# Performance work log

Measured on AMD Instinct MI355X. Metric: run time of the kernel, lower is better.

The kernel has to match this reference:

```python
import jax, jax.numpy as jnp
import numpy as np

L, D, H, N = 9, 256, 4, 1024
DH = D // H          # head dim = 64
FH = DH // 2         # fourier half dim = 32


def _lin(x, W, b):
    return x @ W + b


def _ln(x, g, b, eps=1e-5):
    mu = jnp.mean(x, -1, keepdims=True)
    var = jnp.mean((x - mu) ** 2, -1, keepdims=True)
    return (x - mu) * jax.lax.rsqrt(var + eps) * g + b


def _ffn(x, m, W1, b1, g, beta, W2, b2):
    h = jax.nn.gelu(_ln(_lin(jnp.concatenate([x, m], -1), W1, b1), g, beta), approximate=False)
    return x + _lin(h, W2, b2)


def _rotate_half(x):
    x1, x2 = x[..., 0::2], x[..., 1::2]
    return jnp.stack((-x2, x1), -1).reshape(x.shape)


def _rope(f, t):
    return t * f[0] + _rotate_half(t) * f[1]


def _posenc(kpts, Wr):
    proj = kpts @ Wr                                   # [b,n,FH]
    emb = jnp.stack([jnp.cos(proj), jnp.sin(proj)], 0)  # [2,b,n,FH]
    emb = jnp.repeat(emb, 2, axis=3)                    # [2,b,n,DH]
    return emb[:, None]                                 # [2,1,b,n,DH]


def _heads(t):
    b, n, _ = t.shape
    return t.reshape(b, n, H, DH).transpose(0, 2, 1, 3)


def _merge(t):
    b, h, n, d = t.shape
    return t.transpose(0, 2, 1, 3).reshape(b, n, h * d)


def _self_block(x, enc, Wqkv, bqkv, Wo, bo, fp):
    b, n, _ = x.shape
    qkv = _lin(x, Wqkv, bqkv).reshape(b, n, H, DH, 3).transpose(0, 2, 1, 3, 4)
    q, k, v = qkv[..., 0], qkv[..., 1], qkv[..., 2]
    q, k = _rope(enc, q), _rope(enc, k)
    attn = jax.nn.softmax(jnp.einsum('bhid,bhjd->bhij', q, k) * DH ** -0.5, -1)
    msg = _lin(_merge(jnp.einsum('bhij,bhjd->bhid', attn, v)), Wo, bo)
    return _ffn(x, msg, *fp)


def _cross_block(x0, x1, Wqk, bqk, Wv, bv, Wo, bo, fp):
    s = DH ** -0.25
    qk0 = _heads(_lin(x0, Wqk, bqk)) * s
    qk1 = _heads(_lin(x1, Wqk, bqk)) * s
    v0, v1 = _heads(_lin(x0, Wv, bv)), _heads(_lin(x1, Wv, bv))
    sim = jnp.einsum('bhid,bhjd->bhij', qk0, qk1)       # shared similarity
    m0 = jnp.einsum('bhij,bhjd->bhid', jax.nn.softmax(sim, -1), v1)
    m1 = jnp.einsum('bhij,bhid->bhjd', jax.nn.softmax(sim, -2), v0)
    m0, m1 = _lin(_merge(m0), Wo, bo), _lin(_merge(m1), Wo, bo)
    return _ffn(x0, m0, *fp), _ffn(x1, m1, *fp)


def _assignment(d0, d1, Wp, bp, Wz, bz):
    s = D ** -0.25
    md0, md1 = _lin(d0, Wp, bp) * s, _lin(d1, Wp, bp) * s
    sim = jnp.einsum('bmd,bnd->bmn', md0, md1)
    z0 = d0 @ Wz + bz[:1]                               # [b,m,1]
    z1 = d1 @ Wz + bz[:1]                               # [b,n,1]
    cert = jax.nn.log_sigmoid(z0) + jnp.swapaxes(jax.nn.log_sigmoid(z1), 1, 2)
    inner = jax.nn.log_softmax(sim, -1) + jax.nn.log_softmax(sim, -2) + cert
    col = jax.nn.log_sigmoid(-z0)                       # [b,m,1]
    row = jnp.swapaxes(jax.nn.log_sigmoid(-z1), 1, 2)   # [b,1,n]
    top = jnp.concatenate([inner, col], 2)
    bot = jnp.concatenate([row, jnp.zeros_like(row[:, :, :1])], 2)
    return jnp.concatenate([top, bot], 1)               # [b,m+1,n+1]


def _forward(desc0, desc1, kpts0, kpts1, Wr,
             sWqkv, sbqkv, sWo, sbo, sfW1, sfb1, sfg, sfbeta, sfW2, sfb2,
             cWqk, cbqk, cWv, cbv, cWo, cbo, cfW1, cfb1, cfg, cfbeta, cfW2, cfb2,
             mWp, mbp, mWz, mbz):
    enc0, enc1 = _posenc(kpts0, Wr), _posenc(kpts1, Wr)
    for i in range(L):
        sfp = (sfW1[i], sfb1[i], sfg[i], sfbeta[i], sfW2[i], sfb2[i])
        cfp = (cfW1[i], cfb1[i], cfg[i], cfbeta[i], cfW2[i], cfb2[i])
        desc0 = _self_block(desc0, enc0, sWqkv[i], sbqkv[i], sWo[i], sbo[i], sfp)
        desc1 = _self_block(desc1, enc1, sWqkv[i], sbqkv[i], sWo[i], sbo[i], sfp)
        desc0, desc1 = _cross_block(desc0, desc1, cWqk[i], cbqk[i], cWv[i], cbv[i], cWo[i], cbo[i], cfp)
    return _assignment(desc0, desc1, mWp, mbp, mWz, mbz)


def setup_inputs() -> dict:
    key = jax.random.key(0)
    ks = iter(jax.random.split(key, 64))

    def nrm(shape, std=0.02):
        return std * jax.random.normal(next(ks), shape, jnp.float32)

    return {
        'desc0': nrm((1, N, D), 1.0), 'desc1': nrm((1, N, D), 1.0),
        'kpts0': nrm((1, N, 2), 1.0), 'kpts1': nrm((1, N, 2), 1.0),
        'Wr': nrm((2, FH), 1.0),
        'sWqkv': nrm((L, D, 3 * D)), 'sbqkv': jnp.zeros((L, 3 * D), jnp.float32),
        'sWo': nrm((L, D, D)), 'sbo': jnp.zeros((L, D), jnp.float32),
        'sfW1': nrm((L, 2 * D, 2 * D)), 'sfb1': jnp.zeros((L, 2 * D), jnp.float32),
        'sfg': jnp.ones((L, 2 * D), jnp.float32), 'sfbeta': jnp.zeros((L, 2 * D), jnp.float32),
        'sfW2': nrm((L, 2 * D, D)), 'sfb2': jnp.zeros((L, D), jnp.float32),
        'cWqk': nrm((L, D, D)), 'cbqk': jnp.zeros((L, D), jnp.float32),
        'cWv': nrm((L, D, D)), 'cbv': jnp.zeros((L, D), jnp.float32),
        'cWo': nrm((L, D, D)), 'cbo': jnp.zeros((L, D), jnp.float32),
        'cfW1': nrm((L, 2 * D, 2 * D)), 'cfb1': jnp.zeros((L, 2 * D), jnp.float32),
        'cfg': jnp.ones((L, 2 * D), jnp.float32), 'cfbeta': jnp.zeros((L, 2 * D), jnp.float32),
        'cfW2': nrm((L, 2 * D, D)), 'cfb2': jnp.zeros((L, D), jnp.float32),
        'mWp': nrm((D, D)), 'mbp': jnp.zeros((D,), jnp.float32),
        'mWz': nrm((D, 1)), 'mbz': jnp.zeros((D,), jnp.float32),
    }


def reference(desc0, desc1, kpts0, kpts1, Wr,
              sWqkv, sbqkv, sWo, sbo, sfW1, sfb1, sfg, sfbeta, sfW2, sfb2,
              cWqk, cbqk, cWv, cbv, cWo, cbo, cfW1, cfb1, cfg, cfbeta, cfW2, cfb2,
              mWp, mbp, mWz, mbz):
    return _forward(desc0, desc1, kpts0, kpts1, Wr,
                    sWqkv, sbqkv, sWo, sbo, sfW1, sfb1, sfg, sfbeta, sfW2, sfb2,
                    cWqk, cbqk, cWv, cbv, cWo, cbo, cfW1, cfb1, cfg, cfbeta, cfW2, cfb2,
                    mWp, mbp, mWz, mbz)
```

## Files before the change

kernel.cpp:

```cpp
#include <hip/hip_runtime.h>
#include <cmath>

#define NTOK 1024
#define DM   256
#define NH   4
#define DH   64
#define NL   9

typedef __attribute__((ext_vector_type(8))) __bf16 bf16x8;
typedef __attribute__((ext_vector_type(4))) __bf16 bf16x4;
typedef __attribute__((ext_vector_type(4))) float  f32x4;

__device__ __forceinline__ float logsigf(float x) {
    return fminf(x, 0.0f) - log1pf(expf(-fabsf(x)));
}

__device__ __forceinline__ __bf16 f2bf(float f) {
    unsigned u = __float_as_uint(f);
    u = (u + 0x7FFFu + ((u >> 16) & 1u)) >> 16;
    unsigned short s = (unsigned short)u;
    return __builtin_bit_cast(__bf16, s);
}

__global__ __launch_bounds__(256) void wtrans_all_k(
    const float* __restrict__ sWqkv, const float* __restrict__ sWo,
    const float* __restrict__ sfW1,  const float* __restrict__ sfW2,
    const float* __restrict__ cWqk,  const float* __restrict__ cWv,
    const float* __restrict__ cWo,   const float* __restrict__ cfW1,
    const float* __restrict__ cfW2,  const float* __restrict__ mWp,
    __bf16* __restrict__ wb)
{
    const int z = blockIdx.z;
    const float* src; __bf16* dst; int K, N, b;
    if      (z <  9) { src = sWqkv; dst = wb;            K = 256; N = 768; b = z;      }
    else if (z < 18) { src = sWo;   dst = wb + 1769472;  K = 256; N = 256; b = z - 9;  }
    else if (z < 27) { src = sfW1;  dst = wb + 2359296;  K = 512; N = 512; b = z - 18; }
    else if (z < 36) { src = sfW2;  dst = wb + 4718592;  K = 512; N = 256; b = z - 27; }
    else if (z < 45) { src = cWqk;  dst = wb + 5898240;  K = 256; N = 256; b = z - 36; }
    else if (z < 54) { src = cWv;   dst = wb + 6488064;  K = 256; N = 256; b = z - 45; }
    else if (z < 63) { src = cWo;   dst = wb + 7077888;  K = 256; N = 256; b = z - 54; }
    else if (z < 72) { src = cfW1;  dst = wb + 7667712;  K = 512; N = 512; b = z - 63; }
    else if (z < 81) { src = cfW2;  dst = wb + 10027008; K = 512; N = 256; b = z - 72; }
    else             { src = mWp;   dst = wb + 11206656; K = 256; N = 256; b = 0;      }
    const int n0 = blockIdx.x * 32, k0 = blockIdx.y * 32;
    if (n0 >= N || k0 >= K) return;
    src += (size_t)b * K * N;
    dst += (size_t)b * K * N;

    __shared__ __bf16 t[32][36];
    const int tx = threadIdx.x & 31, ty = threadIdx.x >> 5;
    #pragma unroll
    for (int i = 0; i < 4; ++i) {
        int k = ty + i * 8;
        t[tx][k] = f2bf(src[(size_t)(k0 + k) * N + n0 + tx]);
    }
    __syncthreads();
    const int nr = threadIdx.x >> 3, kc = (threadIdx.x & 7) * 4;
    bf16x4 v = *(const bf16x4*)&t[nr][kc];
    int outr = n0 + nr;
    if (z < 9) {
        int h = outr / 192, r = outr % 192;
        outr = (r % 3) * 256 + h * 64 + (r / 3);
    }
    *(bf16x4*)&dst[(size_t)outr * K + k0 + kc] = v;
}

__global__ __launch_bounds__(256) void wfuse_k(
    const __bf16* __restrict__ tW1s, const __bf16* __restrict__ tWos,
    const __bf16* __restrict__ tW1c, const __bf16* __restrict__ tWoc,
    __bf16* __restrict__ tW1f)
{
    const int z = blockIdx.z, bx = blockIdx.x, tid = threadIdx.x;
    const __bf16* A  = (z < 9) ? tW1s + (size_t)z * 262144 : tW1c + (size_t)(z - 9) * 262144;
    const __bf16* B  = (z < 9) ? tWos + (size_t)z * 65536  : tWoc + (size_t)(z - 9) * 65536;
    __bf16* dst      = tW1f + (size_t)z * 262144;
    const int row0 = blockIdx.y * 32;

    if (bx < 4) {
        const int row = tid >> 3, kc = (tid & 7) * 8;
        bf16x8 v = *(const bf16x8*)&A[(size_t)(row0 + row) * 512 + bx * 64 + kc];
        *(bf16x8*)&dst[(size_t)(row0 + row) * 512 + bx * 64 + kc] = v;
        return;
    }

    __shared__ __bf16 As[8][32][40];
    __shared__ __bf16 Bs[8][64][40];
    const int w = tid >> 6, l = tid & 63;
    const int col0 = (bx - 4) * 64;
    const int wr = (w >> 1) * 16, wc = (w & 1) * 32;
    f32x4 acc0 = {0.f, 0.f, 0.f, 0.f};
    f32x4 acc1 = {0.f, 0.f, 0.f, 0.f};

    const int ar = tid >> 3, ac = (tid & 7) * 4;
    const int tnr = tid >> 3, tkc = (tid & 7) * 8;

    #pragma unroll
    for (int c = 0; c < 8; ++c) {
        bf16x4 av = *(const bf16x4*)&A[(size_t)(row0 + ar) * 512 + 256 + c * 32 + ac];
        *(bf16x4*)&As[c][ar][ac] = av;
        bf16x8 bv = *(const bf16x8*)&B[(size_t)(c * 32 + tnr) * 256 + col0 + tkc];
        #pragma unroll
        for (int e = 0; e < 8; ++e) Bs[c][tkc + e][tnr] = bv[e];
    }
    __syncthreads();
    #pragma unroll
    for (int c = 0; c < 8; ++c) {
        bf16x8 af  = *(const bf16x8*)&As[c][wr + (l & 15)][(l >> 4) * 8];
        bf16x8 bf0 = *(const bf16x8*)&Bs[c][wc + (l & 15)][(l >> 4) * 8];
        bf16x8 bf1 = *(const bf16x8*)&Bs[c][wc + 16 + (l & 15)][(l >> 4) * 8];
        acc0 = __builtin_amdgcn_mfma_f32_16x16x32_bf16(af, bf0, acc0, 0, 0, 0);
        acc1 = __builtin_amdgcn_mfma_f32_16x16x32_bf16(af, bf1, acc1, 0, 0, 0);
    }
    #pragma unroll
    for (int t2 = 0; t2 < 2; ++t2) {
        f32x4 a = t2 ? acc1 : acc0;
        int cc = col0 + wc + t2 * 16 + (l & 15);
        #pragma unroll
        for (int rg = 0; rg < 4; ++rg) {
            int rr = row0 + wr + (l >> 4) * 4 + rg;
            dst[(size_t)rr * 512 + 256 + cc] = f2bf(a[rg]);
        }
    }
}

__global__ __launch_bounds__(256) void bfuse_k(
    const float* __restrict__ sbo, const float* __restrict__ sfW1,
    const float* __restrict__ sfb1, const float* __restrict__ cbo,
    const float* __restrict__ cfW1, const float* __restrict__ cfb1,
    float* __restrict__ bf)
{
    const int z = blockIdx.y;
    const float* bo = (z < 9) ? sbo + z * 256 : cbo + (z - 9) * 256;
    const float* W1 = (z < 9) ? sfW1 + (size_t)z * 262144 : cfW1 + (size_t)(z - 9) * 262144;
    const float* b1 = (z < 9) ? sfb1 + z * 512 : cfb1 + (z - 9) * 512;
    const int o = blockIdx.x * 256 + threadIdx.x;
    float acc = 0.f;
    for (int m = 0; m < 256; ++m)
        acc += bo[m] * W1[(size_t)(256 + m) * 512 + o];
    bf[(size_t)z * 512 + o] = b1[o] + acc;
}

__global__ __launch_bounds__(256) void gemm_qkv_k(
    const __bf16* __restrict__ Ab, const __bf16* __restrict__ Bt,
    const float* __restrict__ bias,
    const float* __restrict__ encc, const float* __restrict__ encs,
    __bf16* __restrict__ qh, __bf16* __restrict__ kh, __bf16* __restrict__ vh)
{
    __shared__ __bf16 As[8][32][40];
    __shared__ __bf16 Bs[8][64][40];
    const int tid = threadIdx.x;
    const int w = tid >> 6, l = tid & 63;
    const int row0 = blockIdx.y * 32, col0 = blockIdx.x * 64;
    const int wr = (w >> 1) * 16, wc = (w & 1) * 32;
    const int quad = l >> 4, l16 = l & 15;
    f32x4 acc0 = {0.f, 0.f, 0.f, 0.f};
    f32x4 acc1 = {0.f, 0.f, 0.f, 0.f};

    const int ar = tid >> 3, ac = (tid & 7) * 4;
    const int bnr = tid >> 2, bkc = (tid & 3) * 8;

    #pragma unroll
    for (int c = 0; c < 8; ++c) {
        const int k0 = c * 32;
        bf16x4 av = *(const bf16x4*)&Ab[(size_t)(row0 + ar) * 256 + k0 + ac];
        *(bf16x4*)&As[c][ar][ac] = av;
        bf16x8 bv = *(const bf16x8*)&Bt[(size_t)(col0 + bnr) * 256 + k0 + bkc];
        *(bf16x8*)&Bs[c][bnr][bkc] = bv;
    }
    __syncthreads();
    #pragma unroll
    for (int c = 0; c < 8; ++c) {
        bf16x8 af  = *(const bf16x8*)&As[c][wr + l16][quad * 8];
        bf16x8 bf0 = *(const bf16x8*)&Bs[c][wc + l16][quad * 8];
        bf16x8 bf1 = *(const bf16x8*)&Bs[c][wc + 16 + l16][quad * 8];
        acc0 = __builtin_amdgcn_mfma_f32_16x16x32_bf16(af, bf0, acc0, 0, 0, 0);
        acc1 = __builtin_amdgcn_mfma_f32_16x16x32_bf16(af, bf1, acc1, 0, 0, 0);
    }

    const int typ = col0 >> 8;
    const int hh  = (col0 & 255) >> 6;
    __bf16* dst = (typ == 0) ? qh : (typ == 1) ? kh : vh;
    #pragma unroll
    for (int t2 = 0; t2 < 2; ++t2) {
        f32x4 a = t2 ? acc1 : acc0;
        const int d = wc + t2 * 16 + l16;
        const float bvv = bias[hh * 192 + d * 3 + typ];
        float full[4], pair[4];
        #pragma unroll
        for (int rg = 0; rg < 4; ++rg) full[rg] = a[rg] + bvv;
        #pragma unroll
        for (int rg = 0; rg < 4; ++rg) pair[rg] = __shfl_xor(full[rg], 1);
        const float sgn = (d & 1) ? 1.0f : -1.0f;
        #pragma unroll
        for (int rg = 0; rg < 4; ++rg) {
            int rr = row0 + wr + quad * 4 + rg;
            float outv;
            if (typ == 2) {
                outv = full[rg];
            } else {
                float c = encc[(size_t)rr * 64 + d];
                float s = encs[(size_t)rr * 64 + d];
                outv = full[rg] * c + sgn * pair[rg] * s;
            }
            int im = rr >> 10, n = rr & 1023;
            dst[(((size_t)(im * 4 + hh)) * 1024 + n) * 64 + d] = f2bf(outv);
        }
    }
}

__global__ __launch_bounds__(256) void gemm_bf_k(
    const __bf16* __restrict__ Ab, const __bf16* __restrict__ A1b,
    const __bf16* __restrict__ Bt, const float* __restrict__ bias,
    float* __restrict__ C, int K, int Nn, int ldc, float scale)
{
    __shared__ __bf16 As[8][32][40];
    __shared__ __bf16 Bs[8][64][40];
    const int tid = threadIdx.x;
    const int w = tid >> 6, l = tid & 63;
    const int row0 = blockIdx.y * 32, col0 = blockIdx.x * 64;
    const int wr = (w >> 1) * 16, wc = (w & 1) * 32;
    f32x4 acc0 = {0.f, 0.f, 0.f, 0.f};
    f32x4 acc1 = {0.f, 0.f, 0.f, 0.f};

    const int ar = tid >> 3, ac = (tid & 7) * 4;
    const int bnr = tid >> 2, bkc = (tid & 3) * 8;

    for (int p0 = 0; p0 < K; p0 += 256) {
        #pragma unroll
        for (int c = 0; c < 8; ++c) {
            const int k0 = p0 + c * 32;
            const int kk = k0 + ac;
            const __bf16* src = (A1b && kk >= 256)
                ? &A1b[(size_t)(row0 + ar) * 256 + (kk - 256)]
                : &Ab[(size_t)(row0 + ar) * 256 + kk];
            bf16x4 av = *(const bf16x4*)src;
            *(bf16x4*)&As[c][ar][ac] = av;
            bf16x8 bv = *(const bf16x8*)&Bt[(size_t)(col0 + bnr) * K + k0 + bkc];
            *(bf16x8*)&Bs[c][bnr][bkc] = bv;
        }
        __syncthreads();
        #pragma unroll
        for (int c = 0; c < 8; ++c) {
            bf16x8 af  = *(const bf16x8*)&As[c][wr + (l & 15)][(l >> 4) * 8];
            bf16x8 bf0 = *(const bf16x8*)&Bs[c][wc + (l & 15)][(l >> 4) * 8];
            bf16x8 bf1 = *(const bf16x8*)&Bs[c][wc + 16 + (l & 15)][(l >> 4) * 8];
            acc0 = __builtin_amdgcn_mfma_f32_16x16x32_bf16(af, bf0, acc0, 0, 0, 0);
            acc1 = __builtin_amdgcn_mfma_f32_16x16x32_bf16(af, bf1, acc1, 0, 0, 0);
        }
        __syncthreads();
    }

    #pragma unroll
    for (int t2 = 0; t2 < 2; ++t2) {
        f32x4 a = t2 ? acc1 : acc0;
        int cc = col0 + wc + t2 * 16 + (l & 15);
        float bvv = bias ? bias[cc] : 0.0f;
        #pragma unroll
        for (int rg = 0; rg < 4; ++rg) {
            int rr = row0 + wr + (l >> 4) * 4 + rg;
            C[(size_t)rr * ldc + cc] = (a[rg] + bvv) * scale;
        }
    }
}

__global__ __launch_bounds__(256) void gemm_bfb_k(
    const __bf16* __restrict__ Ab, const __bf16* __restrict__ Bt,
    const float* __restrict__ bias, __bf16* __restrict__ Cb, float scale)
{
    __shared__ __bf16 As[8][32][40];
    __shared__ __bf16 Bs[8][64][40];
    const int tid = threadIdx.x;
    const int w = tid >> 6, l = tid & 63;
    const int row0 = blockIdx.y * 32, col0 = blockIdx.x * 64;
    const int wr = (w >> 1) * 16, wc = (w & 1) * 32;
    f32x4 acc0 = {0.f, 0.f, 0.f, 0.f};
    f32x4 acc1 = {0.f, 0.f, 0.f, 0.f};

    const int ar = tid >> 3, ac = (tid & 7) * 4;
    const int bnr = tid >> 2, bkc = (tid & 3) * 8;

    #pragma unroll
    for (int c = 0; c < 8; ++c) {
        const int k0 = c * 32;
        bf16x4 av = *(const bf16x4*)&Ab[(size_t)(row0 + ar) * 256 + k0 + ac];
        *(bf16x4*)&As[c][ar][ac] = av;
        bf16x8 bv = *(const bf16x8*)&Bt[(size_t)(col0 + bnr) * 256 + k0 + bkc];
        *(bf16x8*)&Bs[c][bnr][bkc] = bv;
    }
    __syncthreads();
    #pragma unroll
    for (int c = 0; c < 8; ++c) {
        bf16x8 af  = *(const bf16x8*)&As[c][wr + (l & 15)][(l >> 4) * 8];
        bf16x8 bf0 = *(const bf16x8*)&Bs[c][wc + (l & 15)][(l >> 4) * 8];
        bf16x8 bf1 = *(const bf16x8*)&Bs[c][wc + 16 + (l & 15)][(l >> 4) * 8];
        acc0 = __builtin_amdgcn_mfma_f32_16x16x32_bf16(af, bf0, acc0, 0, 0, 0);
        acc1 = __builtin_amdgcn_mfma_f32_16x16x32_bf16(af, bf1, acc1, 0, 0, 0);
    }

    #pragma unroll
    for (int t2 = 0; t2 < 2; ++t2) {
        f32x4 a = t2 ? acc1 : acc0;
        int cc = col0 + wc + t2 * 16 + (l & 15);
        float bvv = bias[cc];
        #pragma unroll
        for (int rg = 0; rg < 4; ++rg) {
            int rr = row0 + wr + (l >> 4) * 4 + rg;
            Cb[(size_t)rr * 256 + cc] = f2bf((a[rg] + bvv) * scale);
        }
    }
}

__global__ __launch_bounds__(256) void gemm_bfa_k(
    const __bf16* __restrict__ Ab, const __bf16* __restrict__ Bt,
    const float* __restrict__ bias, const float* __restrict__ R,
    float* __restrict__ C, __bf16* __restrict__ Cb, int Nn)
{
    __shared__ __bf16 As[8][32][40];
    __shared__ __bf16 Bs[8][64][40];
    const int tid = threadIdx.x;
    const int w = tid >> 6, l = tid & 63;
    const int row0 = blockIdx.y * 32, col0 = blockIdx.x * 64;
    const int wr = (w >> 1) * 16, wc = (w & 1) * 32;
    f32x4 acc0 = {0.f, 0.f, 0.f, 0.f};
    f32x4 acc1 = {0.f, 0.f, 0.f, 0.f};

    const int ar = tid >> 3, ac = (tid & 7) * 4;
    const int bnr = tid >> 2, bkc = (tid & 3) * 8;

    for (int p0 = 0; p0 < 512; p0 += 256) {
        #pragma unroll
        for (int c = 0; c < 8; ++c) {
            const int k0 = p0 + c * 32;
            bf16x4 av = *(const bf16x4*)&Ab[(size_t)(row0 + ar) * 512 + k0 + ac];
            *(bf16x4*)&As[c][ar][ac] = av;
            bf16x8 bv = *(const bf16x8*)&Bt[(size_t)(col0 + bnr) * 512 + k0 + bkc];
            *(bf16x8*)&Bs[c][bnr][bkc] = bv;
        }
        __syncthreads();
        #pragma unroll
        for (int c = 0; c < 8; ++c) {
            bf16x8 af  = *(const bf16x8*)&As[c][wr + (l & 15)][(l >> 4) * 8];
            bf16x8 bf0 = *(const bf16x8*)&Bs[c][wc + (l & 15)][(l >> 4) * 8];
            bf16x8 bf1 = *(const bf16x8*)&Bs[c][wc + 16 + (l & 15)][(l >> 4) * 8];
            acc0 = __builtin_amdgcn_mfma_f32_16x16x32_bf16(af, bf0, acc0, 0, 0, 0);
            acc1 = __builtin_amdgcn_mfma_f32_16x16x32_bf16(af, bf1, acc1, 0, 0, 0);
        }
        __syncthreads();
    }

    #pragma unroll
    for (int t2 = 0; t2 < 2; ++t2) {
        f32x4 a = t2 ? acc1 : acc0;
        int cc = col0 + wc + t2 * 16 + (l & 15);
        float bvv = bias[cc];
        #pragma unroll
        for (int rg = 0; rg < 4; ++rg) {
            int rr = row0 + wr + (l >> 4) * 4 + rg;
            float outv = a[rg] + bvv + R[(size_t)rr * Nn + cc];
            C[(size_t)rr * Nn + cc]  = outv;
            Cb[(size_t)rr * Nn + cc] = f2bf(outv);
        }
    }
}

__global__ __launch_bounds__(256) void gemm_hm2_k(
    const __bf16* __restrict__ Ab, const __bf16* __restrict__ Btq,
    const float* __restrict__ bq, const __bf16* __restrict__ Btv,
    const float* __restrict__ bv, __bf16* __restrict__ outq,
    __bf16* __restrict__ outv, float scaleq)
{
    const int bx = blockIdx.x;
    const __bf16* Bt  = (bx < 4) ? Btq : Btv;
    const float* bias = (bx < 4) ? bq : bv;
    __bf16* C         = (bx < 4) ? outq : outv;
    const float scale = (bx < 4) ? scaleq : 1.0f;

    __shared__ __bf16 As[8][32][40];
    __shared__ __bf16 Bs[8][64][40];
    const int tid = threadIdx.x;
    const int w = tid >> 6, l = tid & 63;
    const int row0 = blockIdx.y * 32, col0 = (bx & 3) * 64;
    const int wr = (w >> 1) * 16, wc = (w & 1) * 32;
    f32x4 acc0 = {0.f, 0.f, 0.f, 0.f};
    f32x4 acc1 = {0.f, 0.f, 0.f, 0.f};

    const int ar = tid >> 3, ac = (tid & 7) * 4;
    const int bnr = tid >> 2, bkc = (tid & 3) * 8;

    #pragma unroll
    for (int c = 0; c < 8; ++c) {
        const int k0 = c * 32;
        bf16x4 av = *(const bf16x4*)&Ab[(size_t)(row0 + ar) * 256 + k0 + ac];
        *(bf16x4*)&As[c][ar][ac] = av;
        bf16x8 bv8 = *(const bf16x8*)&Bt[(size_t)(col0 + bnr) * 256 + k0 + bkc];
        *(bf16x8*)&Bs[c][bnr][bkc] = bv8;
    }
    __syncthreads();
    #pragma unroll
    for (int c = 0; c < 8; ++c) {
        bf16x8 af  = *(const bf16x8*)&As[c][wr + (l & 15)][(l >> 4) * 8];
        bf16x8 bf0 = *(const bf16x8*)&Bs[c][wc + (l & 15)][(l >> 4) * 8];
        bf16x8 bf1 = *(const bf16x8*)&Bs[c][wc + 16 + (l & 15)][(l >> 4) * 8];
        acc0 = __builtin_amdgcn_mfma_f32_16x16x32_bf16(af, bf0, acc0, 0, 0, 0);
        acc1 = __builtin_amdgcn_mfma_f32_16x16x32_bf16(af, bf1, acc1, 0, 0, 0);
    }

    #pragma unroll
    for (int t2 = 0; t2 < 2; ++t2) {
        f32x4 a = t2 ? acc1 : acc0;
        int cc = col0 + wc + t2 * 16 + (l & 15);
        float bvv = bias ? bias[cc] : 0.0f;
        int h = cc >> 6, d = cc & 63;
        #pragma unroll
        for (int rg = 0; rg < 4; ++rg) {
            int rr = row0 + wr + (l >> 4) * 4 + rg;
            int im = rr >> 10, n = rr & 1023;
            C[(((size_t)(im * 4 + h)) * 1024 + n) * 64 + d] = f2bf((a[rg] + bvv) * scale);
        }
    }
}

__global__ __launch_bounds__(256) void gemm_bt_k(
    const __bf16* __restrict__ Ab, const __bf16* __restrict__ Bb,
    float* __restrict__ C, int Nn)
{
    __shared__ __bf16 As[8][32][40];
    __shared__ __bf16 Bs[8][64][40];
    const int tid = threadIdx.x;
    const int w = tid >> 6, l = tid & 63;
    const int row0 = blockIdx.y * 32, col0 = blockIdx.x * 64;
    const int wr = (w >> 1) * 16, wc = (w & 1) * 32;
    f32x4 acc0 = {0.f, 0.f, 0.f, 0.f};
    f32x4 acc1 = {0.f, 0.f, 0.f, 0.f};

    const int ar = tid >> 3, ac = (tid & 7) * 4;
    const int bnr = tid >> 2, bkc = (tid & 3) * 8;

    #pragma unroll
    for (int c = 0; c < 8; ++c) {
        const int k0 = c * 32;
        bf16x4 av = *(const bf16x4*)&Ab[(size_t)(row0 + ar) * 256 + k0 + ac];
        *(bf16x4*)&As[c][ar][ac] = av;
        bf16x8 bv = *(const bf16x8*)&Bb[(size_t)(col0 + bnr) * 256 + k0 + bkc];
        *(bf16x8*)&Bs[c][bnr][bkc] = bv;
    }
    __syncthreads();
    #pragma unroll
    for (int c = 0; c < 8; ++c) {
        bf16x8 af  = *(const bf16x8*)&As[c][wr + (l & 15)][(l >> 4) * 8];
        bf16x8 bf0 = *(const bf16x8*)&Bs[c][wc + (l & 15)][(l >> 4) * 8];
        bf16x8 bf1 = *(const bf16x8*)&Bs[c][wc + 16 + (l & 15)][(l >> 4) * 8];
        acc0 = __builtin_amdgcn_mfma_f32_16x16x32_bf16(af, bf0, acc0, 0, 0, 0);
        acc1 = __builtin_amdgcn_mfma_f32_16x16x32_bf16(af, bf1, acc1, 0, 0, 0);
    }

    #pragma unroll
    for (int t2 = 0; t2 < 2; ++t2) {
        f32x4 a = t2 ? acc1 : acc0;
        int cc = col0 + wc + t2 * 16 + (l & 15);
        #pragma unroll
        for (int rg = 0; rg < 4; ++rg) {
            int rr = row0 + wr + (l >> 4) * 4 + rg;
            C[(size_t)rr * Nn + cc] = a[rg];
        }
    }
}

__global__ __launch_bounds__(256) void init_k(
    const float* __restrict__ desc0, const float* __restrict__ desc1,
    const float* __restrict__ kpts0, const float* __restrict__ kpts1,
    const float* __restrict__ Wr, float* __restrict__ x,
    __bf16* __restrict__ xb,
    float* __restrict__ encc, float* __restrict__ encs)
{
    int idx = blockIdx.x * 256 + threadIdx.x;
    if (idx < 524288) {
        float v = (idx < 262144) ? desc0[idx] : desc1[idx - 262144];
        x[idx]  = v;
        xb[idx] = f2bf(v);
    } else {
        int p = idx - 524288;
        int im = p >> 15, q = p & 32767;
        int i = q >> 5, f = q & 31;
        const float* kp = im ? kpts1 : kpts0;
        float* ec = encc + im * 65536;
        float* es = encs + im * 65536;
        float pr = kp[i * 2] * Wr[f] + kp[i * 2 + 1] * Wr[32 + f];
        float c = cosf(pr), s = sinf(pr);
        ec[i * 64 + 2 * f] = c; ec[i * 64 + 2 * f + 1] = c;
        es[i * 64 + 2 * f] = s; es[i * 64 + 2 * f + 1] = s;
    }
}

__global__ __launch_bounds__(256) void attn_k(
    const __bf16* __restrict__ Qg, const __bf16* __restrict__ Kg,
    const __bf16* __restrict__ Vg, __bf16* __restrict__ out,
    float scale, int cross)
{
    const int qt = blockIdx.x, hv = blockIdx.y;
    const int kvh = cross ? (hv ^ 4) : hv;
    const int tid = threadIdx.x;
    const int w = tid >> 6, lane = tid & 63;
    const int quad = lane >> 4, l16 = lane & 15;
    const int n0 = qt * 16;

    __shared__ __align__(16) char smem[44032];
    char* base = smem + w * 11008;
    __bf16* kb  = (__bf16*)(base);
    __bf16* vtb = (__bf16*)(base + 4608);
    __bf16* ptb = (__bf16*)(base + 9728);

    bf16x8 qf[2];
    {
        const bf16x8* Qp = (const bf16x8*)(Qg + (((size_t)hv * 1024) + n0 + l16) * 64);
        qf[0] = Qp[quad];
        qf[1] = Qp[4 + quad];
    }

    const __bf16* Kbase = Kg + (size_t)kvh * 1024 * 64;
    const __bf16* Vbase = Vg + (size_t)kvh * 1024 * 64;

    float m[4] = {-1e30f, -1e30f, -1e30f, -1e30f};
    float lsum[4] = {0.f, 0.f, 0.f, 0.f};
    f32x4 o[4] = {{0,0,0,0},{0,0,0,0},{0,0,0,0},{0,0,0,0}};

    const int kj = lane >> 1, kd = (lane & 1) * 32;
    const int vjp = lane & 15, vd0 = (lane >> 4) * 16;

    bf16x8 kr[4];
    uint4  vr[4];
    {
        const int j0 = w * 256;
        const bf16x8* kp = (const bf16x8*)(Kbase + (size_t)(j0 + kj) * 64 + kd);
        kr[0] = kp[0]; kr[1] = kp[1]; kr[2] = kp[2]; kr[3] = kp[3];
        const uint4* va = (const uint4*)(Vbase + (size_t)(j0 + 2 * vjp) * 64 + vd0);
        const uint4* vb = (const uint4*)(Vbase + (size_t)(j0 + 2 * vjp + 1) * 64 + vd0);
        vr[0] = va[0]; vr[1] = va[1]; vr[2] = vb[0]; vr[3] = vb[1];
    }

    for (int t = 0; t < 8; ++t) {
        {
            __bf16* krow = kb + kj * 72 + kd;
            *(bf16x8*)(krow)      = kr[0];
            *(bf16x8*)(krow + 8)  = kr[1];
            *(bf16x8*)(krow + 16) = kr[2];
            *(bf16x8*)(krow + 24) = kr[3];
            #pragma unroll
            for (int g = 0; g < 2; ++g) {
                uint4 ua = vr[g], ub = vr[2 + g];
                unsigned au[4] = {ua.x, ua.y, ua.z, ua.w};
                unsigned bu[4] = {ub.x, ub.y, ub.z, ub.w};
                #pragma unroll
                for (int e = 0; e < 4; ++e) {
                    int i = g * 8 + e * 2;
                    unsigned pk0 = ((bu[e] & 0xFFFFu) << 16) | (au[e] & 0xFFFFu);
                    unsigned pk1 = (bu[e] & 0xFFFF0000u) | (au[e] >> 16);
                    *(unsigned*)((char*)vtb + ((vd0 + i) * 40 + 2 * vjp) * 2)     = pk0;
                    *(unsigned*)((char*)vtb + ((vd0 + i + 1) * 40 + 2 * vjp) * 2) = pk1;
                }
            }
        }
        if (t < 7) {
            const int j1 = w * 256 + (t + 1) * 32;
            const bf16x8* kp = (const bf16x8*)(Kbase + (size_t)(j1 + kj) * 64 + kd);
            kr[0] = kp[0]; kr[1] = kp[1]; kr[2] = kp[2]; kr[3] = kp[3];
            const uint4* va = (const uint4*)(Vbase + (size_t)(j1 + 2 * vjp) * 64 + vd0);
            const uint4* vb = (const uint4*)(Vbase + (size_t)(j1 + 2 * vjp + 1) * 64 + vd0);
            vr[0] = va[0]; vr[1] = va[1]; vr[2] = vb[0]; vr[3] = vb[1];
        }

        f32x4 s0 = {0,0,0,0}, s1 = {0,0,0,0};
        #pragma unroll
        for (int kt = 0; kt < 2; ++kt) {
            bf16x8 k0 = *(const bf16x8*)(kb + (0 * 16 + l16) * 72 + kt * 32 + quad * 8);
            bf16x8 k1 = *(const bf16x8*)(kb + (1 * 16 + l16) * 72 + kt * 32 + quad * 8);
            s0 = __builtin_amdgcn_mfma_f32_16x16x32_bf16(qf[kt], k0, s0, 0, 0, 0);
            s1 = __builtin_amdgcn_mfma_f32_16x16x32_bf16(qf[kt], k1, s1, 0, 0, 0);
        }

        float rm[4], p0[4], p1[4], rs[4];
        #pragma unroll
        for (int r = 0; r < 4; ++r) {
            s0[r] *= scale; s1[r] *= scale;
            rm[r] = fmaxf(s0[r], s1[r]);
        }
        #pragma unroll
        for (int ofs = 1; ofs < 16; ofs <<= 1)
            #pragma unroll
            for (int r = 0; r < 4; ++r)
                rm[r] = fmaxf(rm[r], __shfl_xor(rm[r], ofs));
        #pragma unroll
        for (int r = 0; r < 4; ++r) {
            float mn = fmaxf(m[r], rm[r]);
            float alpha = __expf(m[r] - mn);
            m[r] = mn;
            p0[r] = __expf(s0[r] - mn);
            p1[r] = __expf(s1[r] - mn);
            rs[r] = p0[r] + p1[r];
            lsum[r] *= alpha;
            #pragma unroll
            for (int dt = 0; dt < 4; ++dt) o[dt][r] *= alpha;
        }
        #pragma unroll
        for (int ofs = 1; ofs < 16; ofs <<= 1)
            #pragma unroll
            for (int r = 0; r < 4; ++r)
                rs[r] += __shfl_xor(rs[r], ofs);
        #pragma unroll
        for (int r = 0; r < 4; ++r) lsum[r] += rs[r];

        #pragma unroll
        for (int r = 0; r < 4; ++r) {
            ptb[(quad * 4 + r) * 40 + l16]      = f2bf(p0[r]);
            ptb[(quad * 4 + r) * 40 + 16 + l16] = f2bf(p1[r]);
        }
        bf16x8 pf = *(const bf16x8*)(ptb + l16 * 40 + quad * 8);
        #pragma unroll
        for (int dt = 0; dt < 4; ++dt) {
            bf16x8 vf = *(const bf16x8*)(vtb + (dt * 16 + l16) * 40 + quad * 8);
            o[dt] = __builtin_amdgcn_mfma_f32_16x16x32_bf16(pf, vf, o[dt], 0, 0, 0);
        }
    }

    __syncthreads();
    float* Om = (float*)smem;
    float* mm = Om + 4096;
    float* lm = mm + 64;
    #pragma unroll
    for (int dt = 0; dt < 4; ++dt)
        #pragma unroll
        for (int r = 0; r < 4; ++r)
            Om[(w * 16 + quad * 4 + r) * 64 + dt * 16 + l16] = o[dt][r];
    if (l16 == 0) {
        #pragma unroll
        for (int r = 0; r < 4; ++r) {
            mm[w * 16 + quad * 4 + r] = m[r];
            lm[w * 16 + quad * 4 + r] = lsum[r];
        }
    }
    __syncthreads();

    const int q = tid >> 4, dg = tid & 15;
    float M = -1e30f;
    #pragma unroll
    for (int w2 = 0; w2 < 4; ++w2) M = fmaxf(M, mm[w2 * 16 + q]);
    float L = 0.f;
    float4 acc = {0.f, 0.f, 0.f, 0.f};
    #pragma unroll
    for (int w2 = 0; w2 < 4; ++w2) {
        float e = __expf(mm[w2 * 16 + q] - M);
        L += e * lm[w2 * 16 + q];
        float4 ov = *(const float4*)&Om[(w2 * 16 + q) * 64 + dg * 4];
        acc.x += e * ov.x; acc.y += e * ov.y; acc.z += e * ov.z; acc.w += e * ov.w;
    }
    float inv = 1.0f / L;
    bf16x4 ob;
    ob[0] = f2bf(acc.x * inv); ob[1] = f2bf(acc.y * inv);
    ob[2] = f2bf(acc.z * inv); ob[3] = f2bf(acc.w * inv);
    int row = (hv >> 2) * 1024 + n0 + q;
    *(bf16x4*)&out[(size_t)row * 256 + (hv & 3) * 64 + dg * 4] = ob;
}

__global__ __launch_bounds__(256) void lngelu_k(
    const float* __restrict__ x, __bf16* __restrict__ outb,
    const float* __restrict__ g, const float* __restrict__ beta)
{
    int row = blockIdx.x * 4 + (threadIdx.x >> 6);
    int lane = threadIdx.x & 63;
    const float* xr = x + (size_t)row * 512;
    __bf16* ob = outb + (size_t)row * 512;
    float4 v0 = *(const float4*)&xr[lane * 4];
    float4 v1 = *(const float4*)&xr[256 + lane * 4];
    float s = v0.x + v0.y + v0.z + v0.w + v1.x + v1.y + v1.z + v1.w;
    #pragma unroll
    for (int ofs = 1; ofs < 64; ofs <<= 1) s += __shfl_xor(s, ofs);
    float mu = s * (1.0f / 512.0f);
    float d0x = v0.x - mu, d0y = v0.y - mu, d0z = v0.z - mu, d0w = v0.w - mu;
    float d1x = v1.x - mu, d1y = v1.y - mu, d1z = v1.z - mu, d1w = v1.w - mu;
    float vv = d0x*d0x + d0y*d0y + d0z*d0z + d0w*d0w
             + d1x*d1x + d1y*d1y + d1z*d1z + d1w*d1w;
    #pragma unroll
    for (int ofs = 1; ofs < 64; ofs <<= 1) vv += __shfl_xor(vv, ofs);
    float rstd = rsqrtf(vv * (1.0f / 512.0f) + 1e-5f);
    const float IS2 = 0.70710678118654752f;
    bf16x4 o0, o1;
    {
        float4 gg = *(const float4*)&g[lane * 4];
        float4 bb = *(const float4*)&beta[lane * 4];
        float y;
        y = d0x * rstd * gg.x + bb.x; o0[0] = f2bf(0.5f * y * (1.0f + erff(y * IS2)));
        y = d0y * rstd * gg.y + bb.y; o0[1] = f2bf(0.5f * y * (1.0f + erff(y * IS2)));
        y = d0z * rstd * gg.z + bb.z; o0[2] = f2bf(0.5f * y * (1.0f + erff(y * IS2)));
        y = d0w * rstd * gg.w + bb.w; o0[3] = f2bf(0.5f * y * (1.0f + erff(y * IS2)));
    }
    {
        float4 gg = *(const float4*)&g[256 + lane * 4];
        float4 bb = *(const float4*)&beta[256 + lane * 4];
        float y;
        y = d1x * rstd * gg.x + bb.x; o1[0] = f2bf(0.5f * y * (1.0f + erff(y * IS2)));
        y = d1y * rstd * gg.y + bb.y; o1[1] = f2bf(0.5f * y * (1.0f + erff(y * IS2)));
        y = d1z * rstd * gg.z + bb.z; o1[2] = f2bf(0.5f * y * (1.0f + erff(y * IS2)));
        y = d1w * rstd * gg.w + bb.w; o1[3] = f2bf(0.5f * y * (1.0f + erff(y * IS2)));
    }
    *(bf16x4*)&ob[lane * 4]       = o0;
    *(bf16x4*)&ob[256 + lane * 4] = o1;
}

__global__ __launch_bounds__(256) void z_k(
    const float* __restrict__ x, const float* __restrict__ Wz,
    const float* __restrict__ bz, float* __restrict__ z)
{
    int row = blockIdx.x * 4 + (threadIdx.x >> 6);
    int lane = threadIdx.x & 63;
    float4 v  = *(const float4*)&x[(size_t)row * 256 + lane * 4];
    float4 wv = *(const float4*)&Wz[lane * 4];
    float s = v.x * wv.x + v.y * wv.y + v.z * wv.z + v.w * wv.w;
    #pragma unroll
    for (int ofs = 1; ofs < 64; ofs <<= 1) s += __shfl_xor(s, ofs);
    if (lane == 0) z[row] = s + bz[0];
}

__global__ __launch_bounds__(256) void lse_k(
    const float* __restrict__ sim, float* __restrict__ rls,
    float* __restrict__ cls)
{
    const int b = blockIdx.x, t = threadIdx.x;
    const int isCol = b >> 10, rc = b & 1023;
    const size_t base = isCol ? (size_t)rc : (size_t)rc * 1024;
    const size_t stride = isCol ? 1024 : 1;
    __shared__ float red[256];
    float mx = -1e30f;
    for (int j = t; j < NTOK; j += 256) mx = fmaxf(mx, sim[base + stride * j]);
    red[t] = mx; __syncthreads();
    for (int s = 128; s > 0; s >>= 1) {
        if (t < s) red[t] = fmaxf(red[t], red[t + s]);
        __syncthreads();
    }
    mx = red[0]; __syncthreads();
    float sum = 0.0f;
    for (int j = t; j < NTOK; j += 256) sum += expf(sim[base + stride * j] - mx);
    red[t] = sum; __syncthreads();
    for (int s = 128; s > 0; s >>= 1) {
        if (t < s) red[t] += red[t + s];
        __syncthreads();
    }
    if (t == 0) (isCol ? cls : rls)[rc] = mx + logf(red[0]);
}

__global__ __launch_bounds__(256) void assemble_k(
    const float* __restrict__ sim, const float* __restrict__ rls,
    const float* __restrict__ cls, const float* __restrict__ z0,
    const float* __restrict__ z1, float* __restrict__ out)
{
    int idx = blockIdx.x * 256 + threadIdx.x;
    const int W = NTOK + 1;
    if (idx >= W * W) return;
    int i = idx / W, j = idx % W;
    float v;
    if (i < NTOK && j < NTOK) {
        v = 2.0f * sim[(size_t)i * NTOK + j] - rls[i] - cls[j] + logsigf(z0[i]) + logsigf(z1[j]);
    } else if (i < NTOK) {
        v = logsigf(-z0[i]);
    } else if (j < NTOK) {
        v = logsigf(-z1[j]);
    } else {
        v = 0.0f;
    }
    out[idx] = v;
}

extern "C" void kernel_launch(void* const* d_in, const int* in_sizes, int n_in,
                              void* d_out, int out_size, void* d_ws, size_t ws_size,
                              hipStream_t stream)
{
    const float* desc0 = (const float*)d_in[0];
    const float* desc1 = (const float*)d_in[1];
    const float* kpts0 = (const float*)d_in[2];
    const float* kpts1 = (const float*)d_in[3];
    const float* Wr    = (const float*)d_in[4];
    const float* sWqkv = (const float*)d_in[5];
    const float* sbqkv = (const float*)d_in[6];
    const float* sWo   = (const float*)d_in[7];
    const float* sbo   = (const float*)d_in[8];
    const float* sfW1  = (const float*)d_in[9];
    const float* sfb1  = (const float*)d_in[10];
    const float* sfg   = (const float*)d_in[11];
    const float* sfbt  = (const float*)d_in[12];
    const float* sfW2  = (const float*)d_in[13];
    const float* sfb2  = (const float*)d_in[14];
    const float* cWqk  = (const float*)d_in[15];
    const float* cbqk  = (const float*)d_in[16];
    const float* cWv   = (const float*)d_in[17];
    const float* cbv   = (const float*)d_in[18];
    const float* cWo   = (const float*)d_in[19];
    const float* cbo   = (const float*)d_in[20];
    const float* cfW1  = (const float*)d_in[21];
    const float* cfb1  = (const float*)d_in[22];
    const float* cfg   = (const float*)d_in[23];
    const float* cfbt  = (const float*)d_in[24];
    const float* cfW2  = (const float*)d_in[25];
    const float* cfb2  = (const float*)d_in[26];
    const float* mWp   = (const float*)d_in[27];
    const float* mbp   = (const float*)d_in[28];
    const float* mWz   = (const float*)d_in[29];
    const float* mbz   = (const float*)d_in[30];

    float* ws = (float*)d_ws;
    float*  x    = ws;
    float*  encc = ws + 524288;
    float*  encs = ws + 655360;
    float*  pre  = ws + 786432;
    __bf16* preb = (__bf16*)(ws + 1835008);
    __bf16* qh   = (__bf16*)(ws + 2359296);
    __bf16* kh   = (__bf16*)(ws + 2621440);
    __bf16* vh   = (__bf16*)(ws + 2883584);
    __bf16* msgb = (__bf16*)(ws + 3145728);
    float*  zb   = ws + 3276800;
    float*  rlsb = ws + 3278848;
    float*  clsb = ws + 3279872;
    float*  sim  = pre;
    __bf16* mdb  = (__bf16*)(ws + 1835008);

    __bf16* wb    = (__bf16*)(ws + 3280896);
    __bf16* tWqkv = wb;
    __bf16* tWo   = tWqkv + 1769472;
    __bf16* tW1   = tWo   + 589824;
    __bf16* tW2   = tW1   + 2359296;
    __bf16* tcQk  = tW2   + 1179648;
    __bf16* tcV   = tcQk  + 589824;
    __bf16* tcWo  = tcV   + 589824;
    __bf16* tcW1  = tcWo  + 589824;
    __bf16* tcW2  = tcW1  + 2359296;
    __bf16* tmWp  = tcW2  + 1179648;
    __bf16* tW1f  = (__bf16*)(ws + 8916992);
    float*  bfb   = ws + 11276288;
    __bf16* xb    = (__bf16*)(ws + 11285504);

    wtrans_all_k<<<dim3(24, 16, 82), 256, 0, stream>>>(
        sWqkv, sWo, sfW1, sfW2, cWqk, cWv, cWo, cfW1, cfW2, mWp, wb);
    wfuse_k<<<dim3(8, 16, 18), 256, 0, stream>>>(tW1, tWo, tcW1, tcWo, tW1f);
    bfuse_k<<<dim3(2, 18), 256, 0, stream>>>(sbo, sfW1, sfb1, cbo, cfW1, cfb1, bfb);

    const float SELF_SCALE  = 0.125f;
    const float CROSS_SCALE = 0.35355339059327373f;

    init_k<<<2304, 256, 0, stream>>>(desc0, desc1, kpts0, kpts1, Wr, x, xb, encc, encs);

    for (int l = 0; l < NL; ++l) {
        gemm_qkv_k<<<dim3(12, 64), 256, 0, stream>>>(
            xb, tWqkv + (size_t)l * 196608, sbqkv + (size_t)l * 768,
            encc, encs, qh, kh, vh);
        attn_k<<<dim3(64, 8), 256, 0, stream>>>(qh, kh, vh, msgb, SELF_SCALE, 0);
        gemm_bf_k<<<dim3(8, 64), 256, 0, stream>>>(
            xb, msgb, tW1f + (size_t)l * 262144, bfb + (size_t)l * 512,
            pre, 512, 512, 512, 1.0f);
        lngelu_k<<<512, 256, 0, stream>>>(pre, preb, sfg + (size_t)l * 512, sfbt + (size_t)l * 512);
        gemm_bfa_k<<<dim3(4, 64), 256, 0, stream>>>(
            preb, tW2 + (size_t)l * 131072, sfb2 + (size_t)l * 256, x, x, xb, 256);

        gemm_hm2_k<<<dim3(8, 64), 256, 0, stream>>>(
            xb, tcQk + (size_t)l * 65536, cbqk + (size_t)l * 256,
            tcV + (size_t)l * 65536, cbv + (size_t)l * 256,
            qh, vh, CROSS_SCALE);
        attn_k<<<dim3(64, 8), 256, 0, stream>>>(qh, qh, vh, msgb, 1.0f, 1);
        gemm_bf_k<<<dim3(8, 64), 256, 0, stream>>>(
            xb, msgb, tW1f + (size_t)(9 + l) * 262144, bfb + (size_t)(9 + l) * 512,
            pre, 512, 512, 512, 1.0f);
        lngelu_k<<<512, 256, 0, stream>>>(pre, preb, cfg + (size_t)l * 512, cfbt + (size_t)l * 512);
        gemm_bfa_k<<<dim3(4, 64), 256, 0, stream>>>(
            preb, tcW2 + (size_t)l * 131072, cfb2 + (size_t)l * 256, x, x, xb, 256);
    }

    const float MD_SCALE = 0.25f;
    gemm_bfb_k<<<dim3(4, 64), 256, 0, stream>>>(xb, tmWp, mbp, mdb, MD_SCALE);
    z_k<<<512, 256, 0, stream>>>(x, mWz, mbz, zb);
    gemm_bt_k<<<dim3(16, 32), 256, 0, stream>>>(mdb, mdb + 1024 * 256, sim, 1024);
    lse_k<<<2048, 256, 0, stream>>>(sim, rlsb, clsb);
    const int W = NTOK + 1;
    assemble_k<<<(W * W + 255) / 256, 256, 0, stream>>>(sim, rlsb, clsb, zb, zb + 1024, (float*)d_out);
}
```

Measured before the change: 931.5 us.

## Fuse LayerNorm+GELU into second FFN GEMM with full-row tiles

Replaces the separate LayerNorm/GELU kernel and the second FFN GEMM with a single kernel. Each block normalizes 16 rows of the pre-activation, writes the GELU output as bf16 into shared memory, then multiplies against all 256 output columns, reading weights directly from global memory. This removes one launch and the round trip of the bf16 intermediate through memory. In exchange it launches only 128 blocks, and every block re-reads the full weight matrix from global/L2 without shared-memory staging, which may lower occupancy and raise L2 traffic.

```diff
diff --git a/kernel.cpp b/kernel.cpp
--- a/kernel.cpp
+++ b/kernel.cpp
@@ -310,55 +310,94 @@
     }
 }
 
-__global__ __launch_bounds__(256) void gemm_bfa_k(
-    const __bf16* __restrict__ Ab, const __bf16* __restrict__ Bt,
-    const float* __restrict__ bias, const float* __restrict__ R,
-    float* __restrict__ C, __bf16* __restrict__ Cb, int Nn)
-{
-    __shared__ __bf16 As[8][32][40];
-    __shared__ __bf16 Bs[8][64][40];
+__global__ __launch_bounds__(256) void ffn2f_k(
+    const float* __restrict__ pre, const float* __restrict__ g,
+    const float* __restrict__ beta, const __bf16* __restrict__ Bt,
+    const float* __restrict__ bias, float* __restrict__ x,
+    __bf16* __restrict__ xb)
+{
+    __shared__ __bf16 hAs[2][8][16][40];
     const int tid = threadIdx.x;
+    const int r = tid >> 4, sub = tid & 15;
+    const int row0 = blockIdx.x * 16;
+
+    float v[32];
+    const float* pr = pre + (size_t)(row0 + r) * 512 + sub * 32;
+    float s = 0.f;
+    #pragma unroll
+    for (int j4 = 0; j4 < 8; ++j4) {
+        float4 t = *(const float4*)&pr[j4 * 4];
+        v[j4 * 4 + 0] = t.x; v[j4 * 4 + 1] = t.y;
+        v[j4 * 4 + 2] = t.z; v[j4 * 4 + 3] = t.w;
+        s += t.x + t.y + t.z + t.w;
+    }
+    #pragma unroll
+    for (int ofs = 1; ofs < 16; ofs <<= 1) s += __shfl_xor(s, ofs);
+    const float mu = s * (1.0f / 512.0f);
+    float ss = 0.f;
+    #pragma unroll
+    for (int j = 0; j < 32; ++j) { float d = v[j] - mu; ss += d * d; }
+    #pragma unroll
+    for (int ofs = 1; ofs < 16; ofs <<= 1) ss += __shfl_xor(ss, ofs);
+    const float rstd = rsqrtf(ss * (1.0f / 512.0f) + 1e-5f);
+
+    const int p = sub >> 3, c = sub & 7;
+    const float IS2 = 0.70710678118654752f;
+    bf16x8 hb8[4];
+    #pragma unroll
+    for (int j4 = 0; j4 < 8; ++j4) {
+        float4 gg = *(const float4*)&g[sub * 32 + j4 * 4];
+        float4 bb = *(const float4*)&beta[sub * 32 + j4 * 4];
+        float y;
+        y = (v[j4*4+0] - mu) * rstd * gg.x + bb.x;
+        hb8[j4 >> 1][(j4 & 1) * 4 + 0] = f2bf(0.5f * y * (1.0f + erff(y * IS2)));
+        y = (v[j4*4+1] - mu) * rstd * gg.y + bb.y;
+        hb8[j4 >> 1][(j4 & 1) * 4 + 1] = f2bf(0.5f * y * (1.0f + erff(y * IS2)));
+        y = (v[j4*4+2] - mu) * rstd * gg.z + bb.z;
+        hb8[j4 >> 1][(j4 & 1) * 4 + 2] = f2bf(0.5f * y * (1.0f + erff(y * IS2)));
+        y = (v[j4*4+3] - mu) * rstd * gg.w + bb.w;
+        hb8[j4 >> 1][(j4 & 1) * 4 + 3] = f2bf(0.5f * y * (1.0f + erff(y * IS2)));
+    }
+    #pragma unroll
+    for (int j8 = 0; j8 < 4; ++j8)
+        *(bf16x8*)&hAs[p][c][r][j8 * 8] = hb8[j8];
+    __syncthreads();
+
     const int w = tid >> 6, l = tid & 63;
-    const int row0 = blockIdx.y * 32, col0 = blockIdx.x * 64;
-    const int wr = (w >> 1) * 16, wc = (w & 1) * 32;
+    const int quad = l >> 4, l16 = l & 15;
     f32x4 acc0 = {0.f, 0.f, 0.f, 0.f};
     f32x4 acc1 = {0.f, 0.f, 0.f, 0.f};
-
-    const int ar = tid >> 3, ac = (tid & 7) * 4;
-    const int bnr = tid >> 2, bkc = (tid & 3) * 8;
-
-    for (int p0 = 0; p0 < 512; p0 += 256) {
-        #pragma unroll
-        for (int c = 0; c < 8; ++c) {
-            const int k0 = p0 + c * 32;
-            bf16x4 av = *(const bf16x4*)&Ab[(size_t)(row0 + ar) * 512 + k0 + ac];
-            *(bf16x4*)&As[c][ar][ac] = av;
-            bf16x8 bv = *(const bf16x8*)&Bt[(size_t)(col0 + bnr) * 512 + k0 + bkc];
-            *(bf16x8*)&Bs[c][bnr][bkc] = bv;
-        }
-        __syncthreads();
-        #pragma unroll
-        for (int c = 0; c < 8; ++c) {
-            bf16x8 af  = *(const bf16x8*)&As[c][wr + (l & 15)][(l >> 4) * 8];
-            bf16x8 bf0 = *(const bf16x8*)&Bs[c][wc + (l & 15)][(l >> 4) * 8];
-            bf16x8 bf1 = *(const bf16x8*)&Bs[c][wc + 16 + (l & 15)][(l >> 4) * 8];
-            acc0 = __builtin_amdgcn_mfma_f32_16x16x32_bf16(af, bf0, acc0, 0, 0, 0);
-            acc1 = __builtin_amdgcn_mfma_f32_16x16x32_bf16(af, bf1, acc1, 0, 0, 0);
-        }
-        __syncthreads();
-    }
-
-    #pragma unroll
-    for (int t2 = 0; t2 < 2; ++t2) {
-        f32x4 a = t2 ? acc1 : acc0;
-        int cc = col0 + wc + t2 * 16 + (l & 15);
+    f32x4 acc2 = {0.f, 0.f, 0.f, 0.f};
+    f32x4 acc3 = {0.f, 0.f, 0.f, 0.f};
+    const size_t bcol = (size_t)(w * 64 + l16) * 512;
+    #pragma unroll
+    for (int p2 = 0; p2 < 2; ++p2) {
+        #pragma unroll
+        for (int c2 = 0; c2 < 8; ++c2) {
+            bf16x8 af = *(const bf16x8*)&hAs[p2][c2][l16][quad * 8];
+            const size_t kofs = p2 * 256 + c2 * 32 + quad * 8;
+            bf16x8 b0 = *(const bf16x8*)&Bt[bcol + kofs];
+            bf16x8 b1 = *(const bf16x8*)&Bt[bcol + 16 * 512 + kofs];
+            bf16x8 b2 = *(const bf16x8*)&Bt[bcol + 32 * 512 + kofs];
+            bf16x8 b3 = *(const bf16x8*)&Bt[bcol + 48 * 512 + kofs];
+            acc0 = __builtin_amdgcn_mfma_f32_16x16x32_bf16(af, b0, acc0, 0, 0, 0);
+            acc1 = __builtin_amdgcn_mfma_f32_16x16x32_bf16(af, b1, acc1, 0, 0, 0);
+            acc2 = __builtin_amdgcn_mfma_f32_16x16x32_bf16(af, b2, acc2, 0, 0, 0);
+            acc3 = __builtin_amdgcn_mfma_f32_16x16x32_bf16(af, b3, acc3, 0, 0, 0);
+        }
+    }
+
+    #pragma unroll
+    for (int f = 0; f < 4; ++f) {
+        f32x4 a = (f == 0) ? acc0 : (f == 1) ? acc1 : (f == 2) ? acc2 : acc3;
+        int cc = w * 64 + f * 16 + l16;
         float bvv = bias[cc];
         #pragma unroll
         for (int rg = 0; rg < 4; ++rg) {
-            int rr = row0 + wr + (l >> 4) * 4 + rg;
-            float outv = a[rg] + bvv + R[(size_t)rr * Nn + cc];
-            C[(size_t)rr * Nn + cc]  = outv;
-            Cb[(size_t)rr * Nn + cc] = f2bf(outv);
+            int rr = row0 + quad * 4 + rg;
+            float outv = a[rg] + bvv + x[(size_t)rr * 256 + cc];
+            x[(size_t)rr * 256 + cc]  = outv;
+            xb[(size_t)rr * 256 + cc] = f2bf(outv);
         }
     }
 }
@@ -659,51 +698,6 @@
     ob[2] = f2bf(acc.z * inv); ob[3] = f2bf(acc.w * inv);
     int row = (hv >> 2) * 1024 + n0 + q;
     *(bf16x4*)&out[(size_t)row * 256 + (hv & 3) * 64 + dg * 4] = ob;
-}
-
-__global__ __launch_bounds__(256) void lngelu_k(
-    const float* __restrict__ x, __bf16* __restrict__ outb,
-    const float* __restrict__ g, const float* __restrict__ beta)
-{
-    int row = blockIdx.x * 4 + (threadIdx.x >> 6);
-    int lane = threadIdx.x & 63;
-    const float* xr = x + (size_t)row * 512;
-    __bf16* ob = outb + (size_t)row * 512;
-    float4 v0 = *(const float4*)&xr[lane * 4];
-    float4 v1 = *(const float4*)&xr[256 + lane * 4];
-    float s = v0.x + v0.y + v0.z + v0.w + v1.x + v1.y + v1.z + v1.w;
-    #pragma unroll
-    for (int ofs = 1; ofs < 64; ofs <<= 1) s += __shfl_xor(s, ofs);
-    float mu = s * (1.0f / 512.0f);
-    float d0x = v0.x - mu, d0y = v0.y - mu, d0z = v0.z - mu, d0w = v0.w - mu;
-    float d1x = v1.x - mu, d1y = v1.y - mu, d1z = v1.z - mu, d1w = v1.w - mu;
-    float vv = d0x*d0x + d0y*d0y + d0z*d0z + d0w*d0w
-             + d1x*d1x + d1y*d1y + d1z*d1z + d1w*d1w;
-    #pragma unroll
-    for (int ofs = 1; ofs < 64; ofs <<= 1) vv += __shfl_xor(vv, ofs);
-    float rstd = rsqrtf(vv * (1.0f / 512.0f) + 1e-5f);
-    const float IS2 = 0.70710678118654752f;
-    bf16x4 o0, o1;
-    {
-        float4 gg = *(const float4*)&g[lane * 4];
-        float4 bb = *(const float4*)&beta[lane * 4];
-        float y;
-        y = d0x * rstd * gg.x + bb.x; o0[0] = f2bf(0.5f * y * (1.0f + erff(y * IS2)));
-        y = d0y * rstd * gg.y + bb.y; o0[1] = f2bf(0.5f * y * (1.0f + erff(y * IS2)));
-        y = d0z * rstd * gg.z + bb.z; o0[2] = f2bf(0.5f * y * (1.0f + erff(y * IS2)));
-        y = d0w * rstd * gg.w + bb.w; o0[3] = f2bf(0.5f * y * (1.0f + erff(y * IS2)));
-    }
-    {
-        float4 gg = *(const float4*)&g[256 + lane * 4];
-        float4 bb = *(const float4*)&beta[256 + lane * 4];
-        float y;
-        y = d1x * rstd * gg.x + bb.x; o1[0] = f2bf(0.5f * y * (1.0f + erff(y * IS2)));
-        y = d1y * rstd * gg.y + bb.y; o1[1] = f2bf(0.5f * y * (1.0f + erff(y * IS2)));
-        y = d1z * rstd * gg.z + bb.z; o1[2] = f2bf(0.5f * y * (1.0f + erff(y * IS2)));
-        y = d1w * rstd * gg.w + bb.w; o1[3] = f2bf(0.5f * y * (1.0f + erff(y * IS2)));
-    }
-    *(bf16x4*)&ob[lane * 4]       = o0;
-    *(bf16x4*)&ob[256 + lane * 4] = o1;
 }
 
 __global__ __launch_bounds__(256) void z_k(
@@ -810,7 +804,6 @@
     float*  encc = ws + 524288;
     float*  encs = ws + 655360;
     float*  pre  = ws + 786432;
-    __bf16* preb = (__bf16*)(ws + 1835008);
     __bf16* qh   = (__bf16*)(ws + 2359296);
     __bf16* kh   = (__bf16*)(ws + 2621440);
     __bf16* vh   = (__bf16*)(ws + 2883584);
@@ -854,9 +847,9 @@
         gemm_bf_k<<<dim3(8, 64), 256, 0, stream>>>(
             xb, msgb, tW1f + (size_t)l * 262144, bfb + (size_t)l * 512,
             pre, 512, 512, 512, 1.0f);
-        lngelu_k<<<512, 256, 0, stream>>>(pre, preb, sfg + (size_t)l * 512, sfbt + (size_t)l * 512);
-        gemm_bfa_k<<<dim3(4, 64), 256, 0, stream>>>(
-            preb, tW2 + (size_t)l * 131072, sfb2 + (size_t)l * 256, x, x, xb, 256);
+        ffn2f_k<<<128, 256, 0, stream>>>(
+            pre, sfg + (size_t)l * 512, sfbt + (size_t)l * 512,
+            tW2 + (size_t)l * 131072, sfb2 + (size_t)l * 256, x, xb);
 
         gemm_hm2_k<<<dim3(8, 64), 256, 0, stream>>>(
             xb, tcQk + (size_t)l * 65536, cbqk + (size_t)l * 256,
@@ -866,9 +859,9 @@
         gemm_bf_k<<<dim3(8, 64), 256, 0, stream>>>(
             xb, msgb, tW1f + (size_t)(9 + l) * 262144, bfb + (size_t)(9 + l) * 512,
             pre, 512, 512, 512, 1.0f);
-        lngelu_k<<<512, 256, 0, stream>>>(pre, preb, cfg + (size_t)l * 512, cfbt + (size_t)l * 512);
-        gemm_bfa_k<<<dim3(4, 64), 256, 0, stream>>>(
-            preb, tcW2 + (size_t)l * 131072, cfb2 + (size_t)l * 256, x, x, xb, 256);
+        ffn2f_k<<<128, 256, 0, stream>>>(
+            pre, cfg + (size_t)l * 512, cfbt + (size_t)l * 512,
+            tcW2 + (size_t)l * 131072, cfb2 + (size_t)l * 256, x, xb);
     }
 
     const float MD_SCALE = 0.25f;
```

New measurement: 1.110 ms. 1.19x slower.
